# Kernel optimization log

Hardware: AMD Instinct MI355X
Metric: run time of the kernel (lower is better)

The kernel has to match this reference:

```python
import jax, jax.numpy as jnp
import numpy as np

WH, WW = 16, 16          # window size
NUM_HEADS = 6
DIM = 192
N = WH * WW              # tokens per window

def _rel_coords_table():
    # (2*WH-1, 2*WW-1, 2), normalized and scaled by 8 (Swin-V2 style)
    rch = np.arange(-(WH - 1), WH, dtype=np.float32)
    rcw = np.arange(-(WW - 1), WW, dtype=np.float32)
    tab = np.stack(np.meshgrid(rch, rcw, indexing='ij'), axis=-1)
    tab[..., 0] /= (WH - 1)
    tab[..., 1] /= (WW - 1)
    tab *= 8.0
    return tab

def _rel_pos_index():
    # (N, N) int indices into the flattened bias table
    coords = np.stack(np.meshgrid(np.arange(WH), np.arange(WW), indexing='ij'))  # (2,WH,WW)
    cf = coords.reshape(2, -1)                                                   # (2,N)
    rel = cf[:, :, None] - cf[:, None, :]                                        # (2,N,N)
    rel = rel.transpose(1, 2, 0).astype(np.int64)                                # (N,N,2)
    rel[..., 0] += WH - 1
    rel[..., 1] += WW - 1
    rel[..., 0] *= 2 * WW - 1
    return rel.sum(-1)                                                           # (N,N)

_TABLE = jnp.asarray(_rel_coords_table())          # (2WH-1, 2WW-1, 2)
_INDEX = jnp.asarray(_rel_pos_index().reshape(-1)) # (N*N,)

def setup_inputs() -> dict:
    key = jax.random.key(0)
    ks = jax.random.split(key, 8)
    B_ = 256  # num_windows(64) * batch(4)
    return {
        'x': jax.random.normal(ks[0], (B_, N, DIM), dtype=jnp.float32),
        'scale': jax.random.uniform(ks[1], (1, 2), dtype=jnp.float32),
        'mask': jnp.zeros((64, N, N), dtype=jnp.float32),
        'qkv_w': jax.random.normal(ks[2], (3 * DIM, DIM), dtype=jnp.float32) * 0.02,
        'qkv_b': jnp.zeros((3 * DIM,), dtype=jnp.float32),
        'cpb_w1': jax.random.normal(ks[3], (512, 4), dtype=jnp.float32) * 0.02,
        'cpb_b1': jnp.zeros((512,), dtype=jnp.float32),
        'cpb_w2': jax.random.normal(ks[4], (NUM_HEADS, 512), dtype=jnp.float32) * 0.02,
        'cpb_b2': jnp.zeros((NUM_HEADS,), dtype=jnp.float32),
        'proj_w': jax.random.normal(ks[5], (DIM, DIM), dtype=jnp.float32) * 0.02,
        'proj_b': jnp.zeros((DIM,), dtype=jnp.float32),
    }

def reference(x, scale, mask, qkv_w, qkv_b, cpb_w1, cpb_b1, cpb_w2, cpb_b2, proj_w, proj_b):
    B_, n, C = x.shape
    H = NUM_HEADS
    hd = C // H
    qk_scale = hd ** -0.5

    qkv = x @ qkv_w.T + qkv_b                       # (B_, N, 3C)
    qkv = qkv.reshape(B_, n, 3, H, hd).transpose(2, 0, 3, 1, 4)
    q, k, v = qkv[0], qkv[1], qkv[2]                # each (B_, H, N, hd)

    attn = jnp.einsum('bhnd,bhmd->bhnm', q * qk_scale, k)  # (B_, H, N, N)

    # continuous relative position bias: concat table with broadcast scale -> MLP
    rel_cell = jnp.broadcast_to(scale[0], _TABLE.shape[:2] + (2,))    # (2WH-1,2WW-1,2)
    coords4 = jnp.concatenate([_TABLE, rel_cell], axis=-1)            # (...,4)
    hmid = jax.nn.relu(coords4 @ cpb_w1.T + cpb_b1)                   # (...,512)
    table = (hmid @ cpb_w2.T + cpb_b2).reshape(-1, H)                 # (M, H)
    bias = table[_INDEX].reshape(n, n, H).transpose(2, 0, 1)          # (H, N, N)

    attn = attn + bias[None]
    nW = mask.shape[0]
    attn = attn.reshape(B_ // nW, nW, H, n, n) + mask[None, :, None]
    attn = attn.reshape(B_, H, n, n)
    attn = jax.nn.softmax(attn, axis=-1)

    out = jnp.einsum('bhnm,bhmd->bhnd', attn, v)    # (B_, H, N, hd)
    out = out.transpose(0, 2, 1, 3).reshape(B_, n, C)
    return out @ proj_w.T + proj_b
```

## Files before the change

kernel.cpp:

```cpp
#include <hip/hip_runtime.h>
#include <math.h>

#define N_TOK 256
#define NHEADS 6
#define DIM_C 192
#define HD 32
#define B_WIN 256

typedef short bf16x8 __attribute__((ext_vector_type(8)));
typedef float f32x4 __attribute__((ext_vector_type(4)));

__device__ inline short f2bf(float f) {
    unsigned u = __float_as_uint(f);
    u = (u + 0x7fffu + ((u >> 16) & 1u)) >> 16;
    return (short)u;
}
__device__ inline float bf2f(short s) {
    return __uint_as_float(((unsigned)(unsigned short)s) << 16);
}

__global__ __launch_bounds__(512) void cpb_table_kernel(
    const float* __restrict__ scale, const float* __restrict__ w1,
    const float* __restrict__ b1, const float* __restrict__ w2,
    const float* __restrict__ b2, float* __restrict__ table)
{
    __shared__ float red[512];
    const int e = blockIdx.x;
    const int i = e / 31, j = e % 31;
    const float t0 = ((float)(i - 15)) * (8.0f / 15.0f);
    const float t1 = ((float)(j - 15)) * (8.0f / 15.0f);
    const float s0 = scale[0], s1 = scale[1];
    const int t = threadIdx.x;
    const float* w = w1 + t * 4;
    float h = w[0] * t0 + w[1] * t1 + w[2] * s0 + w[3] * s1 + b1[t];
    h = fmaxf(h, 0.0f);
    for (int head = 0; head < NHEADS; ++head) {
        red[t] = h * w2[head * 512 + t];
        __syncthreads();
        for (int s = 256; s > 0; s >>= 1) {
            if (t < s) red[t] += red[t + s];
            __syncthreads();
        }
        if (t == 0) table[e * NHEADS + head] = red[0] + b2[head];
        __syncthreads();
    }
}

__global__ __launch_bounds__(256) void bm_combine_kernel(
    const float* __restrict__ table, const float* __restrict__ mask,
    short* __restrict__ bm)
{
    const size_t g = (size_t)blockIdx.x * 256 + threadIdx.x;
    const int col8 = (int)(g & 31);
    const int row  = (int)((g >> 5) & 255);
    const int bw   = (int)((g >> 13) & 63);
    const int h    = (int)(g >> 19);
    const float4* mp = (const float4*)(mask + ((size_t)bw << 16) + row * 256 + col8 * 8);
    float4 m0 = mp[0], m1 = mp[1];
    float mv[8] = {m0.x, m0.y, m0.z, m0.w, m1.x, m1.y, m1.z, m1.w};
    const int ri = row >> 4, rj = row & 15;
    bf16x8 r;
#pragma unroll
    for (int u = 0; u < 8; ++u) {
        const int col = col8 * 8 + u;
        const int rel0 = ri - (col >> 4) + 15;
        const int rel1 = rj - (col & 15) + 15;
        const float bias = table[(rel0 * 31 + rel1) * NHEADS + h];
        r[u] = f2bf(bias + mv[u]);
    }
    ((bf16x8*)bm)[g] = r;
}

__global__ __launch_bounds__(256) void f32_to_bf16_kernel(
    const float* __restrict__ in, short* __restrict__ out, int n4)
{
    const int i = blockIdx.x * 256 + threadIdx.x;
    if (i < n4) {
        float4 v = ((const float4*)in)[i];
        short4 s;
        s.x = f2bf(v.x); s.y = f2bf(v.y); s.z = f2bf(v.z); s.w = f2bf(v.w);
        ((short4*)out)[i] = s;
    }
}

__global__ __launch_bounds__(256) void qkv_gemm_kernel(
    const short* __restrict__ x16, const short* __restrict__ w16,
    const float* __restrict__ qkv_b,
    short* __restrict__ qb, short* __restrict__ kb, short* __restrict__ vb)
{
    const int t = threadIdx.x;
    const int lane = t & 63;
    const int w = t >> 6;
    const int l15 = lane & 15, quad = lane >> 4;
    const int n0 = blockIdx.x * 64;
    const int m0 = blockIdx.y * 128 + w * 32;

    f32x4 acc[2][4] = {};
#pragma unroll
    for (int ks = 0; ks < 6; ++ks) {
        bf16x8 af[2];
#pragma unroll
        for (int mt = 0; mt < 2; ++mt)
            af[mt] = *(const bf16x8*)(x16 + (size_t)(m0 + mt * 16 + l15) * DIM_C + ks * 32 + quad * 8);
        bf16x8 bfr[4];
#pragma unroll
        for (int nt = 0; nt < 4; ++nt)
            bfr[nt] = *(const bf16x8*)(w16 + (size_t)(n0 + nt * 16 + l15) * DIM_C + ks * 32 + quad * 8);
#pragma unroll
        for (int mt = 0; mt < 2; ++mt)
#pragma unroll
            for (int nt = 0; nt < 4; ++nt)
                acc[mt][nt] = __builtin_amdgcn_mfma_f32_16x16x32_bf16(af[mt], bfr[nt], acc[mt][nt], 0, 0, 0);
    }

    const int which = n0 / DIM_C;
    short* outp = (which == 0) ? qb : (which == 1) ? kb : vb;
    const float qscale = (which == 0) ? 0.17677669529663689f : 1.0f;
#pragma unroll
    for (int mt = 0; mt < 2; ++mt) {
#pragma unroll
        for (int r = 0; r < 4; ++r) {
            const int m = m0 + mt * 16 + quad * 4 + r;
            const int b = m >> 8, tok = m & 255;
#pragma unroll
            for (int nt = 0; nt < 4; ++nt) {
                const int c = n0 + nt * 16 + l15;
                const int rem = c - which * DIM_C;
                const int h = rem >> 5, d = rem & 31;
                const float val = (acc[mt][nt][r] + qkv_b[c]) * qscale;
                outp[((size_t)((b * NHEADS + h) * N_TOK + tok)) * HD + d] = f2bf(val);
            }
        }
    }
}

__global__ __launch_bounds__(256) void proj_gemm_kernel(
    const short* __restrict__ A16, const short* __restrict__ w16,
    const float* __restrict__ proj_b, float* __restrict__ out)
{
    const int t = threadIdx.x;
    const int lane = t & 63;
    const int w = t >> 6;
    const int l15 = lane & 15, quad = lane >> 4;
    const int n0 = blockIdx.x * 64;
    const int m0 = blockIdx.y * 128 + w * 32;

    f32x4 acc[2][4] = {};
#pragma unroll
    for (int ks = 0; ks < 6; ++ks) {
        bf16x8 af[2];
#pragma unroll
        for (int mt = 0; mt < 2; ++mt)
            af[mt] = *(const bf16x8*)(A16 + (size_t)(m0 + mt * 16 + l15) * DIM_C + ks * 32 + quad * 8);
        bf16x8 bfr[4];
#pragma unroll
        for (int nt = 0; nt < 4; ++nt)
            bfr[nt] = *(const bf16x8*)(w16 + (size_t)(n0 + nt * 16 + l15) * DIM_C + ks * 32 + quad * 8);
#pragma unroll
        for (int mt = 0; mt < 2; ++mt)
#pragma unroll
            for (int nt = 0; nt < 4; ++nt)
                acc[mt][nt] = __builtin_amdgcn_mfma_f32_16x16x32_bf16(af[mt], bfr[nt], acc[mt][nt], 0, 0, 0);
    }

#pragma unroll
    for (int mt = 0; mt < 2; ++mt) {
#pragma unroll
        for (int r = 0; r < 4; ++r) {
            const int m = m0 + mt * 16 + quad * 4 + r;
#pragma unroll
            for (int nt = 0; nt < 4; ++nt) {
                const int c = n0 + nt * 16 + l15;
                out[(size_t)m * DIM_C + c] = acc[mt][nt][r] + proj_b[c];
            }
        }
    }
}

#define PS_LD 264

__global__ __launch_bounds__(256, 3) void attn_mfma_kernel(
    const short* __restrict__ q, const short* __restrict__ k,
    const short* __restrict__ v, const short* __restrict__ bm,
    short* __restrict__ out16)
{
    __shared__ __align__(16) short Vt[32][PS_LD];
    __shared__ __align__(16) short Ps[64][PS_LD];
    __shared__ __align__(16) float rowred[64][4];
    __shared__ __align__(16) float rowsum[64][4];

    const int h = blockIdx.x;
    const int b = blockIdx.y;
    const int t = threadIdx.x;
    const int lane = t & 63;
    const int w = t >> 6;
    const int l15 = lane & 15;
    const int quad = lane >> 4;
    const size_t slab = ((size_t)(b * NHEADS + h)) * (N_TOK * HD);

    {
        const bf16x8* vrow = (const bf16x8*)(v + slab + (size_t)t * HD);
#pragma unroll
        for (int u = 0; u < 4; ++u) {
            bf16x8 vv = vrow[u];
#pragma unroll
            for (int j = 0; j < 8; ++j) Vt[u * 8 + j][t] = vv[j];
        }
    }

    bf16x8 kf[4];
#pragma unroll
    for (int nt = 0; nt < 4; ++nt)
        kf[nt] = *(const bf16x8*)(k + slab + (size_t)(w * 64 + nt * 16 + l15) * HD + quad * 8);

    const short* bmB = bm + (((size_t)h * 64 + (b & 63)) << 16);
    const int srow = t >> 2;
    const int scol = (t & 3) * 64;

    __syncthreads();

    for (int chunk = 0; chunk < 4; ++chunk) {
        const int c0 = chunk * 64;

        {
            const bf16x8* src = (const bf16x8*)(bmB + (size_t)(c0 + srow) * 256 + scol);
#pragma unroll
            for (int u = 0; u < 8; ++u)
                *(bf16x8*)&Ps[srow][scol + u * 8] = src[u];
        }

        bf16x8 qf[4];
#pragma unroll
        for (int mt = 0; mt < 4; ++mt)
            qf[mt] = *(const bf16x8*)(q + slab + (size_t)(c0 + mt * 16 + l15) * HD + quad * 8);
        __syncthreads();

        f32x4 S[4][4];
#pragma unroll
        for (int mt = 0; mt < 4; ++mt)
#pragma unroll
            for (int nt = 0; nt < 4; ++nt) {
                f32x4 z = {0.f, 0.f, 0.f, 0.f};
                S[mt][nt] = __builtin_amdgcn_mfma_f32_16x16x32_bf16(qf[mt], kf[nt], z, 0, 0, 0);
            }

#pragma unroll
        for (int mt = 0; mt < 4; ++mt) {
#pragma unroll
            for (int r = 0; r < 4; ++r) {
                const int lrow = mt * 16 + quad * 4 + r;
                float m4 = -1e30f;
#pragma unroll
                for (int nt = 0; nt < 4; ++nt) {
                    float sval = S[mt][nt][r] + bf2f(Ps[lrow][w * 64 + nt * 16 + l15]);
                    S[mt][nt][r] = sval;
                    m4 = fmaxf(m4, sval);
                }
                m4 = fmaxf(m4, __shfl_xor(m4, 1));
                m4 = fmaxf(m4, __shfl_xor(m4, 2));
                m4 = fmaxf(m4, __shfl_xor(m4, 4));
                m4 = fmaxf(m4, __shfl_xor(m4, 8));
                if (l15 == 0) rowred[lrow][w] = m4;
            }
        }
        __syncthreads();

#pragma unroll
        for (int mt = 0; mt < 4; ++mt) {
#pragma unroll
            for (int r = 0; r < 4; ++r) {
                const int lrow = mt * 16 + quad * 4 + r;
                float4 mr = *(const float4*)rowred[lrow];
                const float rm = fmaxf(fmaxf(mr.x, mr.y), fmaxf(mr.z, mr.w));
                float s4 = 0.0f;
#pragma unroll
                for (int nt = 0; nt < 4; ++nt) {
                    const float p = __expf(S[mt][nt][r] - rm);
                    s4 += p;
                    Ps[lrow][w * 64 + nt * 16 + l15] = f2bf(p);
                }
                s4 += __shfl_xor(s4, 1);
                s4 += __shfl_xor(s4, 2);
                s4 += __shfl_xor(s4, 4);
                s4 += __shfl_xor(s4, 8);
                if (l15 == 0) rowsum[lrow][w] = s4;
            }
        }
        __syncthreads();

        f32x4 O0 = {0.f, 0.f, 0.f, 0.f};
        f32x4 O1 = {0.f, 0.f, 0.f, 0.f};
#pragma unroll
        for (int ks = 0; ks < 8; ++ks) {
            bf16x8 af  = *(const bf16x8*)&Ps[w * 16 + l15][ks * 32 + quad * 8];
            bf16x8 bf0 = *(const bf16x8*)&Vt[l15][ks * 32 + quad * 8];
            bf16x8 bf1 = *(const bf16x8*)&Vt[16 + l15][ks * 32 + quad * 8];
            O0 = __builtin_amdgcn_mfma_f32_16x16x32_bf16(af, bf0, O0, 0, 0, 0);
            O1 = __builtin_amdgcn_mfma_f32_16x16x32_bf16(af, bf1, O1, 0, 0, 0);
        }

#pragma unroll
        for (int r = 0; r < 4; ++r) {
            const int lrow = w * 16 + quad * 4 + r;
            float4 sr = *(const float4*)rowsum[lrow];
            const float inv = 1.0f / (sr.x + sr.y + sr.z + sr.w);
            const int token = c0 + lrow;
            short* dst = out16 + ((size_t)(b * N_TOK + token)) * DIM_C + h * HD;
            dst[l15]      = f2bf(O0[r] * inv);
            dst[16 + l15] = f2bf(O1[r] * inv);
        }
        __syncthreads();
    }
}

extern "C" void kernel_launch(void* const* d_in, const int* in_sizes, int n_in,
                              void* d_out, int out_size, void* d_ws, size_t ws_size,
                              hipStream_t stream)
{
    const float* x      = (const float*)d_in[0];
    const float* scale  = (const float*)d_in[1];
    const float* mask   = (const float*)d_in[2];
    const float* qkv_w  = (const float*)d_in[3];
    const float* qkv_b  = (const float*)d_in[4];
    const float* cpb_w1 = (const float*)d_in[5];
    const float* cpb_b1 = (const float*)d_in[6];
    const float* cpb_w2 = (const float*)d_in[7];
    const float* cpb_b2 = (const float*)d_in[8];
    const float* proj_w = (const float*)d_in[9];
    const float* proj_b = (const float*)d_in[10];
    float* out = (float*)d_out;

    const size_t per = (size_t)B_WIN * NHEADS * N_TOK * HD;
    short* wss     = (short*)d_ws;
    short* qb      = wss;
    short* kb      = qb + per;
    short* vb      = kb + per;
    short* ao      = vb + per;
    short* x16     = ao + per;
    short* bmbuf   = x16 + per;
    short* qkvw16  = bmbuf + 25165824;
    short* projw16 = qkvw16 + 110592;
    float* table   = (float*)(projw16 + 36864);

    cpb_table_kernel<<<961, 512, 0, stream>>>(scale, cpb_w1, cpb_b1, cpb_w2, cpb_b2, table);

    bm_combine_kernel<<<(NHEADS * 64 * 256 * 32) / 256, 256, 0, stream>>>(table, mask, bmbuf);

    f32_to_bf16_kernel<<<(int)((per / 4 + 255) / 256), 256, 0, stream>>>(x, x16, (int)(per / 4));
    f32_to_bf16_kernel<<<(110592 / 4 + 255) / 256, 256, 0, stream>>>(qkv_w, qkvw16, 110592 / 4);
    f32_to_bf16_kernel<<<(36864 / 4 + 255) / 256, 256, 0, stream>>>(proj_w, projw16, 36864 / 4);

    qkv_gemm_kernel<<<dim3(9, 512), 256, 0, stream>>>(x16, qkvw16, qkv_b, qb, kb, vb);

    attn_mfma_kernel<<<dim3(NHEADS, B_WIN), 256, 0, stream>>>(qb, kb, vb, bmbuf, ao);

    proj_gemm_kernel<<<dim3(3, 512), 256, 0, stream>>>(ao, projw16, proj_b, out);
}
```

Before: 381.1 us.

## Split bias/mask into MFMA-permuted buffers and give each wave full rows

The old code precombined bias and mask into a 50MB bf16 buffer indexed by head and window. That buffer is replaced by a small per-head bias table and a per-window mask, both stored pre-permuted in the MFMA accumulator layout so each lane reads them directly with vector loads. The attention kernel now gives each wave a full 16-row block across all 256 columns, so the row max and row sum reductions stay inside the wave and the cross-wave shared-memory reductions and most block barriers go away. It also adds XOR swizzling of the LDS tiles to avoid bank conflicts, plus faster bf16 conversion and a hardware reciprocal, at some cost in rounding accuracy.

```diff
diff --git a/kernel.cpp b/kernel.cpp
--- a/kernel.cpp
+++ b/kernel.cpp
@@ -14,6 +14,9 @@
     unsigned u = __float_as_uint(f);
     u = (u + 0x7fffu + ((u >> 16) & 1u)) >> 16;
     return (short)u;
+}
+__device__ inline short f2bf_fast(float f) {
+    return (short)((__float_as_uint(f) + 0x8000u) >> 16);
 }
 __device__ inline float bf2f(short s) {
     return __uint_as_float(((unsigned)(unsigned short)s) << 16);
@@ -46,29 +49,50 @@
     }
 }
 
-__global__ __launch_bounds__(256) void bm_combine_kernel(
-    const float* __restrict__ table, const float* __restrict__ mask,
-    short* __restrict__ bm)
-{
-    const size_t g = (size_t)blockIdx.x * 256 + threadIdx.x;
-    const int col8 = (int)(g & 31);
-    const int row  = (int)((g >> 5) & 255);
-    const int bw   = (int)((g >> 13) & 63);
-    const int h    = (int)(g >> 19);
-    const float4* mp = (const float4*)(mask + ((size_t)bw << 16) + row * 256 + col8 * 8);
-    float4 m0 = mp[0], m1 = mp[1];
-    float mv[8] = {m0.x, m0.y, m0.z, m0.w, m1.x, m1.y, m1.z, m1.w};
-    const int ri = row >> 4, rj = row & 15;
-    bf16x8 r;
-#pragma unroll
-    for (int u = 0; u < 8; ++u) {
-        const int col = col8 * 8 + u;
-        const int rel0 = ri - (col >> 4) + 15;
-        const int rel1 = rj - (col & 15) + 15;
-        const float bias = table[(rel0 * 31 + rel1) * NHEADS + h];
-        r[u] = f2bf(bias + mv[u]);
-    }
-    ((bf16x8*)bm)[g] = r;
+
+__global__ __launch_bounds__(256) void bias_perm_kernel(
+    const float* __restrict__ table, short* __restrict__ bias_p)
+{
+    const int idx8 = blockIdx.x * 256 + threadIdx.x;
+    const int h = idx8 >> 13;
+    const int rem = idx8 & 8191;
+    const int rb = rem >> 9;
+    const int g = (rem >> 6) & 7;
+    const int lane = rem & 63;
+    const int quad = lane >> 4, l15 = lane & 15;
+    bf16x8 o;
+#pragma unroll
+    for (int j = 0; j < 8; ++j) {
+        const int nt = g * 2 + (j >> 2), r = j & 3;
+        const int row = rb * 16 + quad * 4 + r;
+        const int col = nt * 16 + l15;
+        const int rel0 = (row >> 4) - (col >> 4) + 15;
+        const int rel1 = (row & 15) - (col & 15) + 15;
+        o[j] = f2bf(table[(rel0 * 31 + rel1) * NHEADS + h]);
+    }
+    ((bf16x8*)bias_p)[idx8] = o;
+}
+
+__global__ __launch_bounds__(256) void mask_perm_kernel(
+    const float* __restrict__ mask, short* __restrict__ mask_p)
+{
+    const int idx8 = blockIdx.x * 256 + threadIdx.x;
+    const int bw = idx8 >> 13;
+    const int rem = idx8 & 8191;
+    const int rb = rem >> 9;
+    const int g = (rem >> 6) & 7;
+    const int lane = rem & 63;
+    const int quad = lane >> 4, l15 = lane & 15;
+    const float* ms = mask + ((size_t)bw << 16);
+    bf16x8 o;
+#pragma unroll
+    for (int j = 0; j < 8; ++j) {
+        const int nt = g * 2 + (j >> 2), r = j & 3;
+        const int row = rb * 16 + quad * 4 + r;
+        const int col = nt * 16 + l15;
+        o[j] = f2bf(ms[row * 256 + col]);
+    }
+    ((bf16x8*)mask_p)[idx8] = o;
 }
 
 __global__ __launch_bounds__(256) void f32_to_bf16_kernel(
@@ -181,13 +205,11 @@
 
 __global__ __launch_bounds__(256, 3) void attn_mfma_kernel(
     const short* __restrict__ q, const short* __restrict__ k,
-    const short* __restrict__ v, const short* __restrict__ bm,
-    short* __restrict__ out16)
+    const short* __restrict__ v, const short* __restrict__ bias_p,
+    const short* __restrict__ mask_p, short* __restrict__ out16)
 {
     __shared__ __align__(16) short Vt[32][PS_LD];
-    __shared__ __align__(16) short Ps[64][PS_LD];
-    __shared__ __align__(16) float rowred[64][4];
-    __shared__ __align__(16) float rowsum[64][4];
+    __shared__ __align__(16) short Pw[4][16][PS_LD];
 
     const int h = blockIdx.x;
     const int b = blockIdx.y;
@@ -204,112 +226,105 @@
         for (int u = 0; u < 4; ++u) {
             bf16x8 vv = vrow[u];
 #pragma unroll
-            for (int j = 0; j < 8; ++j) Vt[u * 8 + j][t] = vv[j];
-        }
-    }
-
-    bf16x8 kf[4];
-#pragma unroll
-    for (int nt = 0; nt < 4; ++nt)
-        kf[nt] = *(const bf16x8*)(k + slab + (size_t)(w * 64 + nt * 16 + l15) * HD + quad * 8);
-
-    const short* bmB = bm + (((size_t)h * 64 + (b & 63)) << 16);
-    const int srow = t >> 2;
-    const int scol = (t & 3) * 64;
-
+            for (int j = 0; j < 8; ++j) {
+                const int d = u * 8 + j;
+                Vt[d][t ^ (((d >> 3) & 1) * 16)] = vv[j];
+            }
+        }
+    }
     __syncthreads();
 
+    const short* bslab = bias_p + h * 65536;
+    const short* mslab = mask_p + ((b & 63) * 65536);
+
     for (int chunk = 0; chunk < 4; ++chunk) {
-        const int c0 = chunk * 64;
-
-        {
-            const bf16x8* src = (const bf16x8*)(bmB + (size_t)(c0 + srow) * 256 + scol);
-#pragma unroll
-            for (int u = 0; u < 8; ++u)
-                *(bf16x8*)&Ps[srow][scol + u * 8] = src[u];
-        }
-
-        bf16x8 qf[4];
-#pragma unroll
-        for (int mt = 0; mt < 4; ++mt)
-            qf[mt] = *(const bf16x8*)(q + slab + (size_t)(c0 + mt * 16 + l15) * HD + quad * 8);
-        __syncthreads();
-
-        f32x4 S[4][4];
-#pragma unroll
-        for (int mt = 0; mt < 4; ++mt)
-#pragma unroll
-            for (int nt = 0; nt < 4; ++nt) {
-                f32x4 z = {0.f, 0.f, 0.f, 0.f};
-                S[mt][nt] = __builtin_amdgcn_mfma_f32_16x16x32_bf16(qf[mt], kf[nt], z, 0, 0, 0);
-            }
-
-#pragma unroll
-        for (int mt = 0; mt < 4; ++mt) {
+        const int rb = chunk * 4 + w;
+
+        const bf16x8 qf = *(const bf16x8*)(q + slab + (size_t)(rb * 16 + l15) * HD + quad * 8);
+
+        f32x4 S[16];
+#pragma unroll
+        for (int nt = 0; nt < 16; ++nt) {
+            const bf16x8 kf = *(const bf16x8*)(k + slab + (size_t)(nt * 16 + l15) * HD + quad * 8);
+            f32x4 z = {0.f, 0.f, 0.f, 0.f};
+            S[nt] = __builtin_amdgcn_mfma_f32_16x16x32_bf16(qf, kf, z, 0, 0, 0);
+        }
+
+        float mx[4] = {-1e30f, -1e30f, -1e30f, -1e30f};
+#pragma unroll
+        for (int half = 0; half < 2; ++half) {
+            bf16x8 bb[4], mm[4];
+#pragma unroll
+            for (int gg = 0; gg < 4; ++gg) {
+                const int g = half * 4 + gg;
+                const int off = ((rb * 8 + g) * 64 + lane) * 8;
+                bb[gg] = *(const bf16x8*)(bslab + off);
+                mm[gg] = *(const bf16x8*)(mslab + off);
+            }
+#pragma unroll
+            for (int gg = 0; gg < 4; ++gg) {
+#pragma unroll
+                for (int jj = 0; jj < 8; ++jj) {
+                    const int nt = (half * 4 + gg) * 2 + (jj >> 2);
+                    const int r = jj & 3;
+                    const float sv = S[nt][r] + bf2f(bb[gg][jj]) + bf2f(mm[gg][jj]);
+                    S[nt][r] = sv;
+                    mx[r] = fmaxf(mx[r], sv);
+                }
+            }
+        }
+
+#pragma unroll
+        for (int r = 0; r < 4; ++r) {
+            mx[r] = fmaxf(mx[r], __shfl_xor(mx[r], 1));
+            mx[r] = fmaxf(mx[r], __shfl_xor(mx[r], 2));
+            mx[r] = fmaxf(mx[r], __shfl_xor(mx[r], 4));
+            mx[r] = fmaxf(mx[r], __shfl_xor(mx[r], 8));
+        }
+
+        float sm[4] = {0.f, 0.f, 0.f, 0.f};
+#pragma unroll
+        for (int nt = 0; nt < 16; ++nt) {
 #pragma unroll
             for (int r = 0; r < 4; ++r) {
-                const int lrow = mt * 16 + quad * 4 + r;
-                float m4 = -1e30f;
-#pragma unroll
-                for (int nt = 0; nt < 4; ++nt) {
-                    float sval = S[mt][nt][r] + bf2f(Ps[lrow][w * 64 + nt * 16 + l15]);
-                    S[mt][nt][r] = sval;
-                    m4 = fmaxf(m4, sval);
-                }
-                m4 = fmaxf(m4, __shfl_xor(m4, 1));
-                m4 = fmaxf(m4, __shfl_xor(m4, 2));
-                m4 = fmaxf(m4, __shfl_xor(m4, 4));
-                m4 = fmaxf(m4, __shfl_xor(m4, 8));
-                if (l15 == 0) rowred[lrow][w] = m4;
-            }
-        }
-        __syncthreads();
-
-#pragma unroll
-        for (int mt = 0; mt < 4; ++mt) {
-#pragma unroll
-            for (int r = 0; r < 4; ++r) {
-                const int lrow = mt * 16 + quad * 4 + r;
-                float4 mr = *(const float4*)rowred[lrow];
-                const float rm = fmaxf(fmaxf(mr.x, mr.y), fmaxf(mr.z, mr.w));
-                float s4 = 0.0f;
-#pragma unroll
-                for (int nt = 0; nt < 4; ++nt) {
-                    const float p = __expf(S[mt][nt][r] - rm);
-                    s4 += p;
-                    Ps[lrow][w * 64 + nt * 16 + l15] = f2bf(p);
-                }
-                s4 += __shfl_xor(s4, 1);
-                s4 += __shfl_xor(s4, 2);
-                s4 += __shfl_xor(s4, 4);
-                s4 += __shfl_xor(s4, 8);
-                if (l15 == 0) rowsum[lrow][w] = s4;
-            }
-        }
-        __syncthreads();
+                const float p = __expf(S[nt][r] - mx[r]);
+                sm[r] += p;
+                const int lr = quad * 4 + r;
+                Pw[w][lr][(nt * 16 + l15) ^ (((lr >> 3) & 1) * 16)] = f2bf_fast(p);
+            }
+        }
+        float inv[4];
+#pragma unroll
+        for (int r = 0; r < 4; ++r) {
+            sm[r] += __shfl_xor(sm[r], 1);
+            sm[r] += __shfl_xor(sm[r], 2);
+            sm[r] += __shfl_xor(sm[r], 4);
+            sm[r] += __shfl_xor(sm[r], 8);
+            inv[r] = __builtin_amdgcn_rcpf(sm[r]);
+        }
+
+        __asm__ volatile("s_waitcnt lgkmcnt(0)" ::: "memory");
 
         f32x4 O0 = {0.f, 0.f, 0.f, 0.f};
         f32x4 O1 = {0.f, 0.f, 0.f, 0.f};
+        const int sw = ((l15 >> 3) & 1) * 16;
 #pragma unroll
         for (int ks = 0; ks < 8; ++ks) {
-            bf16x8 af  = *(const bf16x8*)&Ps[w * 16 + l15][ks * 32 + quad * 8];
-            bf16x8 bf0 = *(const bf16x8*)&Vt[l15][ks * 32 + quad * 8];
-            bf16x8 bf1 = *(const bf16x8*)&Vt[16 + l15][ks * 32 + quad * 8];
+            const int cb = ks * 32 + quad * 8;
+            bf16x8 af  = *(const bf16x8*)&Pw[w][l15][cb ^ sw];
+            bf16x8 bf0 = *(const bf16x8*)&Vt[l15][cb ^ sw];
+            bf16x8 bf1 = *(const bf16x8*)&Vt[16 + l15][cb ^ sw];
             O0 = __builtin_amdgcn_mfma_f32_16x16x32_bf16(af, bf0, O0, 0, 0, 0);
             O1 = __builtin_amdgcn_mfma_f32_16x16x32_bf16(af, bf1, O1, 0, 0, 0);
         }
 
 #pragma unroll
         for (int r = 0; r < 4; ++r) {
-            const int lrow = w * 16 + quad * 4 + r;
-            float4 sr = *(const float4*)rowsum[lrow];
-            const float inv = 1.0f / (sr.x + sr.y + sr.z + sr.w);
-            const int token = c0 + lrow;
+            const int token = rb * 16 + quad * 4 + r;
             short* dst = out16 + ((size_t)(b * N_TOK + token)) * DIM_C + h * HD;
-            dst[l15]      = f2bf(O0[r] * inv);
-            dst[16 + l15] = f2bf(O1[r] * inv);
-        }
-        __syncthreads();
+            dst[l15]      = f2bf_fast(O0[r] * inv[r]);
+            dst[16 + l15] = f2bf_fast(O1[r] * inv[r]);
+        }
     }
 }
 
@@ -337,14 +352,16 @@
     short* vb      = kb + per;
     short* ao      = vb + per;
     short* x16     = ao + per;
-    short* bmbuf   = x16 + per;
-    short* qkvw16  = bmbuf + 25165824;
+    short* bias_p  = x16 + per;
+    short* mask_p  = bias_p + 393216;
+    short* qkvw16  = mask_p + 4194304;
     short* projw16 = qkvw16 + 110592;
     float* table   = (float*)(projw16 + 36864);
 
     cpb_table_kernel<<<961, 512, 0, stream>>>(scale, cpb_w1, cpb_b1, cpb_w2, cpb_b2, table);
 
-    bm_combine_kernel<<<(NHEADS * 64 * 256 * 32) / 256, 256, 0, stream>>>(table, mask, bmbuf);
+    bias_perm_kernel<<<(NHEADS * 8192) / 256, 256, 0, stream>>>(table, bias_p);
+    mask_perm_kernel<<<(64 * 8192) / 256, 256, 0, stream>>>(mask, mask_p);
 
     f32_to_bf16_kernel<<<(int)((per / 4 + 255) / 256), 256, 0, stream>>>(x, x16, (int)(per / 4));
     f32_to_bf16_kernel<<<(110592 / 4 + 255) / 256, 256, 0, stream>>>(qkv_w, qkvw16, 110592 / 4);
@@ -352,7 +369,7 @@
 
     qkv_gemm_kernel<<<dim3(9, 512), 256, 0, stream>>>(x16, qkvw16, qkv_b, qb, kb, vb);
 
-    attn_mfma_kernel<<<dim3(NHEADS, B_WIN), 256, 0, stream>>>(qb, kb, vb, bmbuf, ao);
+    attn_mfma_kernel<<<dim3(NHEADS, B_WIN), 256, 0, stream>>>(qb, kb, vb, bias_p, mask_p, ao);
 
     proj_gemm_kernel<<<dim3(3, 512), 256, 0, stream>>>(ao, projw16, proj_b, out);
 }
```

New measurement: 361.9 us. -5.0%, faster.
